# Kernel tuning notes

Hardware: AMD Instinct MI355X
Metric: run time of the kernel (lower is better)

The kernel has to match this reference:

```python
import jax, jax.numpy as jnp
import numpy as np

B, N, D = 4, 2048, 1024
G = 256          # group_size
QK = 128         # query_key_dim
H = 2048         # hidden_dim = int(dim * expansion_factor)
LN_EPS = 1e-5


def setup_inputs() -> dict:
    key = jax.random.key(0)
    ks = jax.random.split(key, 6)
    s = 0.02
    return {
        "x": jax.random.normal(ks[0], (B, N, D), jnp.float32),
        "ln_g": jnp.ones((D,), jnp.float32),
        "ln_b": jnp.zeros((D,), jnp.float32),
        "W_hidden": jax.random.normal(ks[1], (D, 2 * H), jnp.float32) * s,
        "b_hidden": jnp.zeros((2 * H,), jnp.float32),
        "W_qk": jax.random.normal(ks[2], (D, QK), jnp.float32) * s,
        "b_qk": jnp.zeros((QK,), jnp.float32),
        "os_gamma": jnp.ones((4, QK), jnp.float32) + jax.random.normal(ks[3], (4, QK), jnp.float32) * 0.02,
        "os_beta": jnp.zeros((4, QK), jnp.float32),
        "W_out": jax.random.normal(ks[4], (H, D), jnp.float32) * s,
        "b_out": jnp.zeros((D,), jnp.float32),
    }


def _rope(x):
    # x: [b, n, d]; rotary over the sequence dim, matching FLASH.rope(x, dim=1)
    n, d = x.shape[-2], x.shape[-1]
    half = d // 2
    pos = jnp.arange(n, dtype=jnp.float32)
    # freq_seq = -arange(half)/half; inv_freq = 10000 ** (-freq_seq)
    inv_freq = jnp.power(10000.0, jnp.arange(half, dtype=jnp.float32) / half)
    sinusoid = pos[:, None] * inv_freq[None, :]            # [n, half]
    sin, cos = jnp.sin(sinusoid), jnp.cos(sinusoid)
    x1, x2 = jnp.split(x, 2, axis=-1)
    return jnp.concatenate([x1 * cos - x2 * sin, x2 * cos + x1 * sin], axis=-1)


def reference(x, ln_g, ln_b, W_hidden, b_hidden, W_qk, b_qk,
              os_gamma, os_beta, W_out, b_out):
    b, n, d = x.shape
    g = G
    # LayerNorm (biased variance, as torch)
    mu = jnp.mean(x, -1, keepdims=True)
    var = jnp.mean(jnp.square(x - mu), -1, keepdims=True)
    normed = (x - mu) / jnp.sqrt(var + LN_EPS) * ln_g + ln_b

    h = jax.nn.silu(normed @ W_hidden + b_hidden)          # [b, n, 2H]
    v, gate = jnp.split(h, 2, axis=-1)                     # [b, n, H] each
    qk = jax.nn.silu(normed @ W_qk + b_qk)                 # [b, n, QK]

    # OffsetScale: 4 heads -> quad_q, lin_q, quad_k, lin_k
    qk4 = qk[..., None, :] * os_gamma + os_beta            # [b, n, 4, QK]
    quad_q, lin_q, quad_k, lin_k = (_rope(qk4[..., i, :]) for i in range(4))

    pad = (-n) % g
    if pad:
        padf = lambda t: jnp.pad(t, ((0, 0), (0, pad), (0, 0)))
        quad_q, quad_k, lin_q, lin_k, v_p = map(padf, (quad_q, quad_k, lin_q, lin_k, v))
    else:
        v_p = v
    grp = lambda t: t.reshape(b, -1, g, t.shape[-1])       # b (g n) d -> b g n d
    quad_q, quad_k, lin_q, lin_k, vg = map(grp, (quad_q, quad_k, lin_q, lin_k, v_p))

    # group-local quadratic attention with ReLU^2
    sim = jnp.einsum('bgid,bgjd->bgij', quad_q, quad_k) / g
    attn = jnp.square(jax.nn.relu(sim))
    quad_out = jnp.einsum('bgij,bgje->bgie', attn, vg)

    # linear global attention (reduced over groups), divided by full seq len n
    lin_kv = jnp.einsum('bgnd,bgne->bde', lin_k, vg) / n
    lin_out = jnp.einsum('bgnd,bde->bgne', lin_q, lin_kv)

    out = (quad_out + lin_out).reshape(b, -1, vg.shape[-1])[:, :n]
    out = gate * out
    return out @ W_out + b_out + x
```

## Files before the change

### kernel.cpp

```cpp
#include <hip/hip_runtime.h>
#include <stdint.h>

typedef __attribute__((ext_vector_type(8))) short bf16x8_t;
typedef __attribute__((ext_vector_type(4))) float f32x4_t;

#define DI __device__ __forceinline__
#define SBAR() asm volatile("s_barrier" ::: "memory")
#define VMW(n) asm volatile("s_waitcnt vmcnt(" #n ")" ::: "memory")

DI unsigned short f2b(float f) {
  union { float f; unsigned int u; } c; c.f = f;
  unsigned int u = c.u + 0x7FFFu + ((c.u >> 16) & 1u);
  return (unsigned short)(u >> 16);
}
DI unsigned int pack2(float lo, float hi) {
  return (unsigned int)f2b(lo) | ((unsigned int)f2b(hi) << 16);
}
DI float b2f(unsigned short h) {
  union { unsigned int u; float f; } c; c.u = ((unsigned int)h) << 16;
  return c.f;
}
DI float silu_f(float z) { return z / (1.0f + __expf(-z)); }

DI void load_lds16(const unsigned short* g, unsigned short* l) {
  __builtin_amdgcn_global_load_lds(
      (const __attribute__((address_space(1))) unsigned int*)g,
      (__attribute__((address_space(3))) unsigned int*)l,
      16, 0, 0);
}

struct PrepP {
  const float *Wh, *Wo, *Wqk, *x, *g, *b;
  unsigned short *WT, *WoT, *normed;
};

__global__ __launch_bounds__(256) void prep_kernel(PrepP p) {
  const int blk = blockIdx.x;
  const int tx = threadIdx.x & 31, ty = threadIdx.x >> 5;
  if (blk < 6272) {
    const float* in; unsigned short* out; int R, C, gx;
    if (blk < 4096)      { in = p.Wh;  out = p.WT;                 R = 1024; C = 4096; gx = blk; }
    else if (blk < 6144) { in = p.Wo;  out = p.WoT;                R = 2048; C = 1024; gx = blk - 4096; }
    else                 { in = p.Wqk; out = p.WT + 4096 * 1024;   R = 1024; C = 128;  gx = blk - 6144; }
    const int xTiles = C >> 5;
    const int c0 = (gx % xTiles) * 32, r0 = (gx / xTiles) * 32;
    __shared__ float tile[32][33];
#pragma unroll
    for (int i = 0; i < 4; ++i)
      tile[ty + 8 * i][tx] = in[(long)(r0 + ty + 8 * i) * C + c0 + tx];
    __syncthreads();
#pragma unroll
    for (int i = 0; i < 4; ++i)
      out[(long)(c0 + ty + 8 * i) * R + r0 + tx] = f2b(tile[tx][ty + 8 * i]);
  } else {
    const int row = blk - 6272, tid = threadIdx.x;
    __shared__ float red[8];
    float4 v = ((const float4*)(p.x + (long)row * 1024))[tid];
    float s = v.x + v.y + v.z + v.w;
    float ss = v.x * v.x + v.y * v.y + v.z * v.z + v.w * v.w;
    for (int o = 32; o > 0; o >>= 1) { s += __shfl_down(s, o); ss += __shfl_down(ss, o); }
    const int wave = tid >> 6, lane = tid & 63;
    if (lane == 0) { red[wave * 2] = s; red[wave * 2 + 1] = ss; }
    __syncthreads();
    if (tid == 0) {
      float S = red[0] + red[2] + red[4] + red[6];
      float SS = red[1] + red[3] + red[5] + red[7];
      float mu = S * (1.0f / 1024.0f);
      float var = SS * (1.0f / 1024.0f) - mu * mu;
      red[0] = mu; red[1] = rsqrtf(var + 1e-5f);
    }
    __syncthreads();
    const float mu = red[0], rstd = red[1];
    float4 gg = ((const float4*)p.g)[tid];
    float4 bb = ((const float4*)p.b)[tid];
    ushort4 o;
    o.x = f2b((v.x - mu) * rstd * gg.x + bb.x);
    o.y = f2b((v.y - mu) * rstd * gg.y + bb.y);
    o.z = f2b((v.z - mu) * rstd * gg.z + bb.z);
    o.w = f2b((v.w - mu) * rstd * gg.w + bb.w);
    ((ushort4*)(p.normed + (long)row * 1024))[tid] = o;
  }
}

__global__ __launch_bounds__(256) void reduce_cvt(
    const unsigned short* __restrict__ part, unsigned short* __restrict__ out) {
  const int idx = blockIdx.x * 256 + threadIdx.x;
  const int b = idx >> 16, i = idx & 65535;
  float4 s = make_float4(0.f, 0.f, 0.f, 0.f);
#pragma unroll
  for (int sl = 0; sl < 8; ++sl) {
    ushort4 v = ((const ushort4*)part)[(long)(b * 8 + sl) * 65536 + i];
    s.x += b2f(v.x); s.y += b2f(v.y); s.z += b2f(v.z); s.w += b2f(v.w);
  }
  ushort4 o;
  o.x = f2b(s.x); o.y = f2b(s.y); o.z = f2b(s.z); o.w = f2b(s.w);
  ((ushort4*)out)[(long)b * 65536 + i] = o;
}

struct G8P {
  const unsigned short* A;
  const unsigned short* B;
  const float* bias;
  const float* bias2;
  const float* gamma;
  const float* beta;
  unsigned short* vTout;
  unsigned short* gateOut;
  unsigned short* qqO;
  unsigned short* lqO;
  unsigned short* qkhO;
  unsigned short* lkTO;
};

__global__ __launch_bounds__(512, 2) void gemm8p(G8P p) {
  extern __shared__ unsigned char lds[];
  const int tid  = threadIdx.x;
  const int lane = tid & 63;
  const int wave = tid >> 6;
  const bool qk = blockIdx.x < 32;
  int bx, by;
  if (qk) { bx = blockIdx.x; by = 16; }
  else    { const int vg = blockIdx.x - 32; bx = vg >> 4; by = vg & 15; }
  const int wm = (wave & 1) * 128;
  const int wn = (wave >> 1) * 64;
  const int lm = lane & 15;
  const int kb = lane >> 4;

  const int rA  = tid >> 2;
  const int kby = ((tid & 3) << 4) ^ (((rA >> 1) & 3) << 4);
  const unsigned short* gA0 = p.A + (long)(bx * 256 + rA) * 1024 + (kby >> 1);
  const unsigned short* gA1 = gA0 + 128 * 1024;
  const unsigned short* gB0 = p.B + (long)(by * 256 + rA) * 1024 + (kby >> 1);
  const unsigned short* gB1 = gB0 + 128 * 1024;

  const int fxor = (kb << 4) ^ (((lm >> 1) & 3) << 4);

  f32x4_t acc[8][4];
#pragma unroll
  for (int i = 0; i < 8; ++i)
#pragma unroll
    for (int j = 0; j < 4; ++j) acc[i][j] = (f32x4_t){0.f, 0.f, 0.f, 0.f};

  auto stageA = [&](int t) {
    unsigned short* l = (unsigned short*)(lds + (t & 3) * 32768 + wave * 1024);
    load_lds16(gA0 + t * 32, l);
    load_lds16(gA1 + t * 32, (unsigned short*)((unsigned char*)l + 8192));
  };
  auto stageB = [&](int t) {
    unsigned short* l = (unsigned short*)(lds + (t & 3) * 32768 + 16384 + wave * 1024);
    load_lds16(gB0 + t * 32, l);
    load_lds16(gB1 + t * 32, (unsigned short*)((unsigned char*)l + 8192));
  };

#pragma unroll
  for (int u = 0; u < 3; ++u) { stageA(u); stageB(u); }
  VMW(8);
  SBAR();

  constexpr int NT = 16;
#pragma unroll 1
  for (int t = 0; t < NT; ++t) {
    const unsigned char* slot = lds + (t & 3) * 32768;
    bf16x8_t bF[4], aF[4];
#pragma unroll
    for (int j = 0; j < 4; ++j)
      bF[j] = *(const bf16x8_t*)(slot + 16384 + (wn + j * 16 + lm) * 64 + fxor);
#pragma unroll
    for (int i = 0; i < 4; ++i)
      aF[i] = *(const bf16x8_t*)(slot + (wm + i * 16 + lm) * 64 + fxor);
    if (t <= NT - 4) stageA(t + 3);
    SBAR();
    __builtin_amdgcn_s_setprio(1);
#pragma unroll
    for (int i = 0; i < 4; ++i)
#pragma unroll
      for (int j = 0; j < 4; ++j)
        acc[i][j] = __builtin_amdgcn_mfma_f32_16x16x32_bf16(aF[i], bF[j], acc[i][j], 0, 0, 0);
    __builtin_amdgcn_s_setprio(0);
    SBAR();
#pragma unroll
    for (int i = 0; i < 4; ++i)
      aF[i] = *(const bf16x8_t*)(slot + (wm + 64 + i * 16 + lm) * 64 + fxor);
    if (t <= NT - 4) stageB(t + 3);
    SBAR();
    __builtin_amdgcn_s_setprio(1);
#pragma unroll
    for (int i = 0; i < 4; ++i)
#pragma unroll
      for (int j = 0; j < 4; ++j)
        acc[i + 4][j] = __builtin_amdgcn_mfma_f32_16x16x32_bf16(aF[i], bF[j], acc[i + 4][j], 0, 0, 0);
    __builtin_amdgcn_s_setprio(0);
    if (t <= NT - 4)      { VMW(8); }
    else if (t == NT - 3) { VMW(4); }
    else if (t == NT - 2) { VMW(0); }
    SBAR();
  }

  if (qk) {
    unsigned short* q16 = (unsigned short*)lds;
    if (wave < 4) {
#pragma unroll
      for (int i = 0; i < 8; ++i) {
        const int rloc = wm + i * 16 + (lane >> 4) * 4;
#pragma unroll
        for (int j = 0; j < 4; ++j) {
          const int cl = wn + j * 16 + lm;
          const float bb = p.bias2[cl];
#pragma unroll
          for (int r = 0; r < 4; ++r)
            q16[(rloc + r) * 136 + cl] = f2b(silu_f(acc[i][j][r] + bb));
        }
      }
    }
    __syncthreads();
    const int j = tid & 63;
    const int rq = tid >> 6;
    const float freq = powf(10000.0f, (float)j * (1.0f / 64.0f));
    float ga[4], gb[4], ea[4], eb[4];
#pragma unroll
    for (int h = 0; h < 4; ++h) {
      ga[h] = p.gamma[h * 128 + j];  gb[h] = p.gamma[h * 128 + 64 + j];
      ea[h] = p.beta[h * 128 + j];   eb[h] = p.beta[h * 128 + 64 + j];
    }
    unsigned short* outs[3] = {p.qqO, p.lqO, p.qkhO};
    for (int rr = 0; rr < 32; ++rr) {
      const int row = rr * 8 + rq;
      const float x1 = b2f(q16[row * 136 + j]);
      const float x2 = b2f(q16[row * 136 + 64 + j]);
      const int tok = bx * 256 + row;
      const int pos = tok & 2047, bidx = tok >> 11;
      const float ang = (float)pos * freq;
      const float sn = sinf(ang), cs = cosf(ang);
#pragma unroll
      for (int h = 0; h < 3; ++h) {
        const float y1 = x1 * ga[h] + ea[h], y2 = x2 * gb[h] + eb[h];
        outs[h][(long)tok * 128 + j] = f2b(y1 * cs - y2 * sn);
        outs[h][(long)tok * 128 + 64 + j] = f2b(y2 * cs + y1 * sn);
      }
      const float y1 = x1 * ga[3] + ea[3], y2 = x2 * gb[3] + eb[3];
      p.lkTO[((long)bidx * 128 + j) * 2048 + pos] = f2b(y1 * cs - y2 * sn);
      p.lkTO[((long)bidx * 128 + 64 + j) * 2048 + pos] = f2b(y2 * cs + y1 * sn);
    }
  } else if (by < 8) {
    unsigned int* Cx = (unsigned int*)lds;
#pragma unroll
    for (int i = 0; i < 8; ++i) {
      const int c0 = (wm + i * 16) / 2 + (lane >> 4) * 2;
#pragma unroll
      for (int j = 0; j < 4; ++j) {
        const int e = wn + j * 16 + lm;
        const float bb = p.bias[by * 256 + e];
        const float s0 = silu_f(acc[i][j][0] + bb);
        const float s1 = silu_f(acc[i][j][1] + bb);
        const float s2 = silu_f(acc[i][j][2] + bb);
        const float s3 = silu_f(acc[i][j][3] + bb);
        const int x = (e & 7) << 2;
        Cx[e * 128 + (c0 ^ x)]     = pack2(s0, s1);
        Cx[e * 128 + (c0 ^ x) + 1] = pack2(s2, s3);
      }
    }
    __syncthreads();
    const int bq = bx >> 3, nloc0 = (bx & 7) * 256, e0g = by * 256;
    unsigned short* dstBase = p.vTout + ((long)(bq * 2048 + e0g)) * 2048 + nloc0;
#pragma unroll
    for (int rep = 0; rep < 16; ++rep) {
      const int flat = rep * 512 + tid;
      const int e = flat >> 5, q = flat & 31;
      uint4 val = *(const uint4*)(Cx + e * 128 + ((q ^ (e & 7)) << 2));
      *(uint4*)(dstBase + (long)e * 2048 + q * 8) = val;
    }
  } else {
#pragma unroll
    for (int i = 0; i < 8; ++i) {
      const int row0 = bx * 256 + wm + i * 16 + (lane >> 4) * 4;
#pragma unroll
      for (int j = 0; j < 4; ++j) {
        const int colg = by * 256 + wn + j * 16 + lm;
        const float bb = p.bias[colg];
#pragma unroll
        for (int r = 0; r < 4; ++r)
          p.gateOut[(long)(row0 + r) * 2048 + colg - 2048] =
              f2b(silu_f(acc[i][j][r] + bb));
      }
    }
  }
}

struct GQLP {
  const unsigned short* attn;
  const unsigned short* vT;
  const unsigned short* lq;
  const unsigned short* lkvT;
  const unsigned short* gateIn;
  unsigned short* outU;
};

__global__ __launch_bounds__(512, 2) void gemmQL(GQLP p) {
  extern __shared__ unsigned char lds[];
  const int tid  = threadIdx.x;
  const int lane = tid & 63;
  const int wave = tid >> 6;
  const int z  = blockIdx.x >> 3;
  const int by = blockIdx.x & 7;
  const int b = z >> 3, g = z & 7;
  const int wm = (wave & 1) * 128;
  const int wn = (wave >> 1) * 64;
  const int lm = lane & 15;
  const int kb = lane >> 4;

  const int rA  = tid >> 2;
  const int kby = ((tid & 3) << 4) ^ (((rA >> 1) & 3) << 4);
  const int swz = kby >> 1;
  const unsigned short* a1 = p.attn + (long)z * 65536 + rA * 256 + swz;
  const unsigned short* a2 = p.lq + ((long)z * 256 + rA) * 128 + swz;
  const unsigned short* b1 = p.vT + (long)b * 4194304 + (long)(by * 256 + rA) * 2048 + g * 256 + swz;
  const unsigned short* b2 = p.lkvT + (long)b * 262144 + (by * 256 + rA) * 128 + swz;
  const int fxor = (kb << 4) ^ (((lm >> 1) & 3) << 4);

  f32x4_t acc[8][4];
#pragma unroll
  for (int i = 0; i < 8; ++i)
#pragma unroll
    for (int j = 0; j < 4; ++j) acc[i][j] = (f32x4_t){0.f, 0.f, 0.f, 0.f};

  auto stageA = [&](int tt) {
    unsigned short* l  = (unsigned short*)(lds + (tt & 3) * 32768 + wave * 1024);
    unsigned short* lh = (unsigned short*)(lds + (tt & 3) * 32768 + wave * 1024 + 8192);
    if (tt < 8) { load_lds16(a1 + tt * 32, l); load_lds16(a1 + 128 * 256 + tt * 32, lh); }
    else { const int k2 = (tt - 8) * 32;
           load_lds16(a2 + k2, l); load_lds16(a2 + 128 * 128 + k2, lh); }
  };
  auto stageB = [&](int tt) {
    unsigned short* l  = (unsigned short*)(lds + (tt & 3) * 32768 + 16384 + wave * 1024);
    unsigned short* lh = (unsigned short*)(lds + (tt & 3) * 32768 + 16384 + wave * 1024 + 8192);
    if (tt < 8) { load_lds16(b1 + tt * 32, l); load_lds16(b1 + 128 * 2048 + tt * 32, lh); }
    else { const int k2 = (tt - 8) * 32;
           load_lds16(b2 + k2, l); load_lds16(b2 + 128 * 128 + k2, lh); }
  };

#pragma unroll
  for (int u = 0; u < 3; ++u) { stageA(u); stageB(u); }
  VMW(8);
  SBAR();

  constexpr int NT = 12;
#pragma unroll 1
  for (int t = 0; t < NT; ++t) {
    const unsigned char* slot = lds + (t & 3) * 32768;
    bf16x8_t bF[4], aF[4];
#pragma unroll
    for (int j = 0; j < 4; ++j)
      bF[j] = *(const bf16x8_t*)(slot + 16384 + (wn + j * 16 + lm) * 64 + fxor);
#pragma unroll
    for (int i = 0; i < 4; ++i)
      aF[i] = *(const bf16x8_t*)(slot + (wm + i * 16 + lm) * 64 + fxor);
    if (t <= NT - 4) stageA(t + 3);
    SBAR();
    __builtin_amdgcn_s_setprio(1);
#pragma unroll
    for (int i = 0; i < 4; ++i)
#pragma unroll
      for (int j = 0; j < 4; ++j)
        acc[i][j] = __builtin_amdgcn_mfma_f32_16x16x32_bf16(aF[i], bF[j], acc[i][j], 0, 0, 0);
    __builtin_amdgcn_s_setprio(0);
    SBAR();
#pragma unroll
    for (int i = 0; i < 4; ++i)
      aF[i] = *(const bf16x8_t*)(slot + (wm + 64 + i * 16 + lm) * 64 + fxor);
    if (t <= NT - 4) stageB(t + 3);
    SBAR();
    __builtin_amdgcn_s_setprio(1);
#pragma unroll
    for (int i = 0; i < 4; ++i)
#pragma unroll
      for (int j = 0; j < 4; ++j)
        acc[i + 4][j] = __builtin_amdgcn_mfma_f32_16x16x32_bf16(aF[i], bF[j], acc[i + 4][j], 0, 0, 0);
    __builtin_amdgcn_s_setprio(0);
    if (t <= NT - 4)      { VMW(8); }
    else if (t == NT - 3) { VMW(4); }
    else if (t == NT - 2) { VMW(0); }
    SBAR();
  }

#pragma unroll
  for (int i = 0; i < 8; ++i) {
    const int row0 = z * 256 + wm + i * 16 + (lane >> 4) * 4;
#pragma unroll
    for (int j = 0; j < 4; ++j) {
      const int col = by * 256 + wn + j * 16 + lm;
#pragma unroll
      for (int r = 0; r < 4; ++r) {
        const long idx = (long)(row0 + r) * 2048 + col;
        p.outU[idx] = f2b(b2f(p.gateIn[idx]) * acc[i][j][r]);
      }
    }
  }
}

struct GWoP {
  const unsigned short* A;
  const unsigned short* B;
  const float* bias;
  const float* xres;
  float* outF;
};

__global__ __launch_bounds__(512, 2) void gemmWo(GWoP p) {
  extern __shared__ unsigned char lds[];
  const int tid  = threadIdx.x;
  const int lane = tid & 63;
  const int wave = tid >> 6;
  const int bx = blockIdx.x >> 3;
  const int by = blockIdx.x & 7;
  const int wm = (wave & 1) * 128;
  const int wn = (wave >> 1) * 32;
  const int lm = lane & 15;
  const int kb = lane >> 4;

  const int rA  = tid >> 2;
  const int kby = ((tid & 3) << 4) ^ (((rA >> 1) & 3) << 4);
  const unsigned short* gA0 = p.A + (long)(bx * 256 + rA) * 2048 + (kby >> 1);
  const unsigned short* gA1 = gA0 + 128 * 2048;
  const unsigned short* gB0 = p.B + (long)(by * 128 + rA) * 2048 + (kby >> 1);
  const int fxor = (kb << 4) ^ (((lm >> 1) & 3) << 4);

  f32x4_t acc[8][2];
#pragma unroll
  for (int i = 0; i < 8; ++i)
#pragma unroll
    for (int j = 0; j < 2; ++j) acc[i][j] = (f32x4_t){0.f, 0.f, 0.f, 0.f};

  auto stageA = [&](int t) {
    unsigned short* l = (unsigned short*)(lds + (t & 3) * 24576 + wave * 1024);
    load_lds16(gA0 + t * 32, l);
    load_lds16(gA1 + t * 32, (unsigned short*)((unsigned char*)l + 8192));
  };
  auto stageB = [&](int t) {
    unsigned short* l = (unsigned short*)(lds + (t & 3) * 24576 + 16384 + wave * 1024);
    load_lds16(gB0 + t * 32, l);
  };

#pragma unroll
  for (int u = 0; u < 3; ++u) { stageA(u); stageB(u); }
  VMW(6);
  SBAR();

  constexpr int NT = 64;
#pragma unroll 1
  for (int t = 0; t < NT; ++t) {
    const unsigned char* slot = lds + (t & 3) * 24576;
    bf16x8_t bF[2], aF[4];
#pragma unroll
    for (int j = 0; j < 2; ++j)
      bF[j] = *(const bf16x8_t*)(slot + 16384 + (wn + j * 16 + lm) * 64 + fxor);
#pragma unroll
    for (int i = 0; i < 4; ++i)
      aF[i] = *(const bf16x8_t*)(slot + (wm + i * 16 + lm) * 64 + fxor);
    if (t <= NT - 4) stageA(t + 3);
    SBAR();
    __builtin_amdgcn_s_setprio(1);
#pragma unroll
    for (int i = 0; i < 4; ++i)
#pragma unroll
      for (int j = 0; j < 2; ++j)
        acc[i][j] = __builtin_amdgcn_mfma_f32_16x16x32_bf16(aF[i], bF[j], acc[i][j], 0, 0, 0);
    __builtin_amdgcn_s_setprio(0);
    SBAR();
#pragma unroll
    for (int i = 0; i < 4; ++i)
      aF[i] = *(const bf16x8_t*)(slot + (wm + 64 + i * 16 + lm) * 64 + fxor);
    if (t <= NT - 4) stageB(t + 3);
    SBAR();
    __builtin_amdgcn_s_setprio(1);
#pragma unroll
    for (int i = 0; i < 4; ++i)
#pragma unroll
      for (int j = 0; j < 2; ++j)
        acc[i + 4][j] = __builtin_amdgcn_mfma_f32_16x16x32_bf16(aF[i], bF[j], acc[i + 4][j], 0, 0, 0);
    __builtin_amdgcn_s_setprio(0);
    if (t <= NT - 4)      { VMW(6); }
    else if (t == NT - 3) { VMW(3); }
    else if (t == NT - 2) { VMW(0); }
    SBAR();
  }

#pragma unroll
  for (int i = 0; i < 8; ++i) {
    const int row0 = bx * 256 + wm + i * 16 + (lane >> 4) * 4;
#pragma unroll
    for (int j = 0; j < 2; ++j) {
      const int col = by * 128 + wn + j * 16 + lm;
      const float bb = p.bias[col];
#pragma unroll
      for (int r = 0; r < 4; ++r) {
        const long idx = (long)(row0 + r) * 1024 + col;
        p.outF[idx] = acc[i][j][r] + bb + p.xres[idx];
      }
    }
  }
}

enum { EPI_ARELU, EPI_PART };

struct GemmP {
  const unsigned short* A;
  const unsigned short* B;
  int K, lda, ldb, ldc, mPerZ;
  long aZ, bZ;
  float scale;
  unsigned short* outU;
};

template <int EPI>
__global__ __launch_bounds__(256, 2) void gemm_bt(GemmP p) {
  __shared__ __align__(16) unsigned char smem[16384];
  unsigned short* As = (unsigned short*)smem;
  unsigned short* Bs = (unsigned short*)(smem + 8192);

  const int tid = threadIdx.x;
  const int lane = tid & 63;
  const int wave = tid >> 6;
  const int bx = blockIdx.x;
  const int by = blockIdx.y;
  const int z = blockIdx.z;

  unsigned short* lA = As + wave * 32 * 32;
  unsigned short* lB = Bs + wave * 32 * 32;
  const int wm = (wave & 1) * 64;
  const int wn = (wave >> 1) * 64;
  const int lm = lane & 15;
  const int kb = lane >> 4;
  const int rowSel = (wave * 32 + (lane >> 2));
  const int colSel = (lane & 3) * 8;

  f32x4_t acc[4][4];
#pragma unroll
  for (int i = 0; i < 4; ++i)
#pragma unroll
    for (int j = 0; j < 4; ++j) acc[i][j] = (f32x4_t){0.f, 0.f, 0.f, 0.f};

  auto kloop = [&](const unsigned short* Ag, const unsigned short* Bg,
                   int lda, int ldb, int ksteps) {
    const int a16 = 16 * lda, b16 = 16 * ldb;
    for (int kt = 0; kt < ksteps; ++kt) {
      load_lds16(Ag, lA);
      load_lds16(Ag + a16, lA + 512);
      load_lds16(Bg, lB);
      load_lds16(Bg + b16, lB + 512);
      Ag += 32; Bg += 32;
      __syncthreads();
      bf16x8_t aF[4], bF[4];
#pragma unroll
      for (int i = 0; i < 4; ++i)
        aF[i] = *(const bf16x8_t*)(As + (wm + i * 16 + lm) * 32 + kb * 8);
#pragma unroll
      for (int j = 0; j < 4; ++j)
        bF[j] = *(const bf16x8_t*)(Bs + (wn + j * 16 + lm) * 32 + kb * 8);
#pragma unroll
      for (int i = 0; i < 4; ++i)
#pragma unroll
        for (int j = 0; j < 4; ++j)
          acc[i][j] = __builtin_amdgcn_mfma_f32_16x16x32_bf16(aF[i], bF[j], acc[i][j], 0, 0, 0);
      __syncthreads();
    }
  };

  if constexpr (EPI == EPI_PART) {
    const int b = z >> 3, s = z & 7;
    kloop(p.A + (long)b * p.aZ + s * 256 + (long)(bx * 128 + rowSel) * p.lda + colSel,
          p.B + (long)b * p.bZ + s * 256 + (long)(by * 128 + rowSel) * p.ldb + colSel,
          p.lda, p.ldb, p.K >> 5);
  } else {
    kloop(p.A + (long)z * p.aZ + (long)(bx * 128 + rowSel) * p.lda + colSel,
          p.B + (long)z * p.bZ + (long)(by * 128 + rowSel) * p.ldb + colSel,
          p.lda, p.ldb, p.K >> 5);
  }

#pragma unroll
  for (int i = 0; i < 4; ++i) {
    const int row0 = bx * 128 + wm + i * 16 + (lane >> 4) * 4;
    long rowg0;
    if constexpr (EPI == EPI_PART) rowg0 = row0;
    else rowg0 = (long)z * p.mPerZ + row0;
#pragma unroll
    for (int j = 0; j < 4; ++j) {
      const int col = by * 128 + wn + j * 16 + lm;
      if constexpr (EPI == EPI_ARELU) {
#pragma unroll
        for (int r = 0; r < 4; ++r) {
          float s = acc[i][j][r] * p.scale;
          s = s > 0.f ? s : 0.f;
          p.outU[(rowg0 + r) * (long)p.ldc + col] = f2b(s * s);
        }
      } else {
        unsigned short* slab = p.outU + (long)z * 262144;
#pragma unroll
        for (int r = 0; r < 4; ++r)
          slab[(rowg0 + r) * (long)p.ldc + col] = f2b(acc[i][j][r] * p.scale);
      }
    }
  }
}

extern "C" void kernel_launch(void* const* d_in, const int* in_sizes, int n_in,
                              void* d_out, int out_size, void* d_ws, size_t ws_size,
                              hipStream_t stream) {
  const float* x        = (const float*)d_in[0];
  const float* ln_g     = (const float*)d_in[1];
  const float* ln_b     = (const float*)d_in[2];
  const float* W_hidden = (const float*)d_in[3];
  const float* b_hidden = (const float*)d_in[4];
  const float* W_qk     = (const float*)d_in[5];
  const float* b_qk     = (const float*)d_in[6];
  const float* os_gamma = (const float*)d_in[7];
  const float* os_beta  = (const float*)d_in[8];
  const float* W_out    = (const float*)d_in[9];
  const float* b_out    = (const float*)d_in[10];
  float* out = (float*)d_out;

  char* w = (char*)d_ws;
  auto ws = [&](size_t bytes) { char* p = w; w += bytes; return (unsigned short*)p; };
  unsigned short* WT     = ws(8650752);
  unsigned short* WoT    = ws(4194304);
  unsigned short* normed = ws(16777216);
  unsigned short* vT     = ws(33554432);
  unsigned short* gate   = ws(33554432);
  unsigned short* qq     = ws(2097152);
  unsigned short* qkh    = ws(2097152);
  unsigned short* lq     = ws(2097152);
  unsigned short* lkT    = ws(2097152);
  unsigned short* attn   = ws(4194304);
  unsigned short* lkvP   = ws(16777216);
  unsigned short* lkvT   = ws(2097152);
  unsigned short* A3     = ws(33554432);

  static bool s_attr = false;
  if (!s_attr) {
    hipFuncSetAttribute((const void*)gemm8p,
                        hipFuncAttributeMaxDynamicSharedMemorySize, 131072);
    hipFuncSetAttribute((const void*)gemmQL,
                        hipFuncAttributeMaxDynamicSharedMemorySize, 131072);
    hipFuncSetAttribute((const void*)gemmWo,
                        hipFuncAttributeMaxDynamicSharedMemorySize, 98304);
    s_attr = true;
  }

  {
    PrepP p{W_hidden, W_out, W_qk, x, ln_g, ln_b, WT, WoT, normed};
    prep_kernel<<<14464, 256, 0, stream>>>(p);
  }
  {
    G8P p{normed, WT, b_hidden, b_qk, os_gamma, os_beta,
          vT, gate, qq, lq, qkh, lkT};
    gemm8p<<<dim3(544, 1, 1), 512, 131072, stream>>>(p);
  }
  {
    GemmP p{}; p.A = qq; p.B = qkh; p.K = 128; p.lda = 128; p.ldb = 128;
    p.ldc = 256; p.mPerZ = 256; p.aZ = 32768; p.bZ = 32768;
    p.scale = 1.f / 256.f; p.outU = attn;
    gemm_bt<EPI_ARELU><<<dim3(2, 2, 32), 256, 0, stream>>>(p);
  }
  {
    GemmP p{}; p.A = vT; p.B = lkT; p.K = 256; p.lda = 2048; p.ldb = 2048;
    p.ldc = 128; p.mPerZ = 2048; p.aZ = 4194304; p.bZ = 262144;
    p.scale = 1.f / 2048.f; p.outU = lkvP;
    gemm_bt<EPI_PART><<<dim3(16, 1, 32), 256, 0, stream>>>(p);
  }
  reduce_cvt<<<1024, 256, 0, stream>>>(lkvP, lkvT);
  {
    GQLP p{attn, vT, lq, lkvT, gate, A3};
    gemmQL<<<dim3(256, 1, 1), 512, 131072, stream>>>(p);
  }
  {
    GWoP p{A3, WoT, b_out, x, out};
    gemmWo<<<dim3(256, 1, 1), 512, 98304, stream>>>(p);
  }
}
```

Measured before the change: 327.0 us.

## Fuse quad-attention scores into projection GEMM via flag wait; swizzle block order

Removes the separate ReLU² attention-score kernel launch. The score tiles are computed by 128 extra blocks appended to the fused projection GEMM, and these blocks spin on a global counter until the 32 qk blocks have written their outputs. The counter is reset by an extra block in the prep kernel. Block-index remappings are also added in the projection, gemmQL and gemmWo kernels to change the tile traversal order for cache locality. The spin-wait relies on the qk blocks being scheduled before or alongside the waiting blocks, which risks deadlock or idle CUs.

```diff
diff --git a/kernel.cpp b/kernel.cpp
--- a/kernel.cpp
+++ b/kernel.cpp
@@ -32,10 +32,15 @@
 struct PrepP {
   const float *Wh, *Wo, *Wqk, *x, *g, *b;
   unsigned short *WT, *WoT, *normed;
+  unsigned int* flag;
 };
 
 __global__ __launch_bounds__(256) void prep_kernel(PrepP p) {
   const int blk = blockIdx.x;
+  if (blk >= 14464) {
+    if (threadIdx.x == 0) *p.flag = 0u;
+    return;
+  }
   const int tx = threadIdx.x & 31, ty = threadIdx.x >> 5;
   if (blk < 6272) {
     const float* in; unsigned short* out; int R, C, gx;
@@ -110,6 +115,8 @@
   unsigned short* lqO;
   unsigned short* qkhO;
   unsigned short* lkTO;
+  unsigned short* attnO;
+  unsigned int* flag;
 };
 
 __global__ __launch_bounds__(512, 2) void gemm8p(G8P p) {
@@ -117,14 +124,80 @@
   const int tid  = threadIdx.x;
   const int lane = tid & 63;
   const int wave = tid >> 6;
+  const int lm = lane & 15;
+  const int kb = lane >> 4;
+  const int fxor = (kb << 4) ^ (((lm >> 1) & 3) << 4);
+
+  if (blockIdx.x >= 544) {
+    const int az = blockIdx.x - 544;
+    const int zz = az >> 2;
+    const int bq = (az >> 1) & 1, bn = az & 1;
+    if (tid == 0) {
+      while (atomicAdd(p.flag, 0u) < 32u) __builtin_amdgcn_s_sleep(2);
+    }
+    __syncthreads();
+    __threadfence();
+    const int r128 = tid >> 2;
+    const int kby2 = ((tid & 3) << 4) ^ (((r128 >> 1) & 3) << 4);
+    const unsigned short* gq = p.qqO  + ((long)zz * 256 + bq * 128 + r128) * 128 + (kby2 >> 1);
+    const unsigned short* gk = p.qkhO + ((long)zz * 256 + bn * 128 + r128) * 128 + (kby2 >> 1);
+#pragma unroll
+    for (int kt = 0; kt < 4; ++kt) {
+      load_lds16(gq + kt * 32, (unsigned short*)(lds + kt * 8192 + wave * 1024));
+      load_lds16(gk + kt * 32, (unsigned short*)(lds + 32768 + kt * 8192 + wave * 1024));
+    }
+    VMW(0);
+    __syncthreads();
+    const int wm2 = (wave & 1) * 64;
+    const int wn2 = (wave >> 1) * 32;
+    f32x4_t ac[4][2];
+#pragma unroll
+    for (int i = 0; i < 4; ++i)
+#pragma unroll
+      for (int j = 0; j < 2; ++j) ac[i][j] = (f32x4_t){0.f, 0.f, 0.f, 0.f};
+#pragma unroll
+    for (int kt = 0; kt < 4; ++kt) {
+      bf16x8_t aF2[4], bF2[2];
+#pragma unroll
+      for (int i = 0; i < 4; ++i)
+        aF2[i] = *(const bf16x8_t*)(lds + kt * 8192 + (wm2 + i * 16 + lm) * 64 + fxor);
+#pragma unroll
+      for (int j = 0; j < 2; ++j)
+        bF2[j] = *(const bf16x8_t*)(lds + 32768 + kt * 8192 + (wn2 + j * 16 + lm) * 64 + fxor);
+#pragma unroll
+      for (int i = 0; i < 4; ++i)
+#pragma unroll
+        for (int j = 0; j < 2; ++j)
+          ac[i][j] = __builtin_amdgcn_mfma_f32_16x16x32_bf16(aF2[i], bF2[j], ac[i][j], 0, 0, 0);
+    }
+    unsigned short* outA = p.attnO + (long)zz * 65536;
+#pragma unroll
+    for (int i = 0; i < 4; ++i) {
+      const int row0 = bq * 128 + wm2 + i * 16 + (lane >> 4) * 4;
+#pragma unroll
+      for (int j = 0; j < 2; ++j) {
+        const int col = bn * 128 + wn2 + j * 16 + lm;
+#pragma unroll
+        for (int r = 0; r < 4; ++r) {
+          float s = ac[i][j][r] * (1.0f / 256.0f);
+          s = s > 0.f ? s : 0.f;
+          outA[(row0 + r) * 256 + col] = f2b(s * s);
+        }
+      }
+    }
+    return;
+  }
+
   const bool qk = blockIdx.x < 32;
   int bx, by;
   if (qk) { bx = blockIdx.x; by = 16; }
-  else    { const int vg = blockIdx.x - 32; bx = vg >> 4; by = vg & 15; }
+  else {
+    const int vg = blockIdx.x - 32;
+    const int vgs = (vg & 7) * 64 + (vg >> 3);
+    bx = vgs >> 4; by = vgs & 15;
+  }
   const int wm = (wave & 1) * 128;
   const int wn = (wave >> 1) * 64;
-  const int lm = lane & 15;
-  const int kb = lane >> 4;
 
   const int rA  = tid >> 2;
   const int kby = ((tid & 3) << 4) ^ (((rA >> 1) & 3) << 4);
@@ -132,8 +205,6 @@
   const unsigned short* gA1 = gA0 + 128 * 1024;
   const unsigned short* gB0 = p.B + (long)(by * 256 + rA) * 1024 + (kby >> 1);
   const unsigned short* gB1 = gB0 + 128 * 1024;
-
-  const int fxor = (kb << 4) ^ (((lm >> 1) & 3) << 4);
 
   f32x4_t acc[8][4];
 #pragma unroll
@@ -241,6 +312,9 @@
       p.lkTO[((long)bidx * 128 + j) * 2048 + pos] = f2b(y1 * cs - y2 * sn);
       p.lkTO[((long)bidx * 128 + 64 + j) * 2048 + pos] = f2b(y2 * cs + y1 * sn);
     }
+    __threadfence();
+    __syncthreads();
+    if (tid == 0) atomicAdd(p.flag, 1u);
   } else if (by < 8) {
     unsigned int* Cx = (unsigned int*)lds;
 #pragma unroll
@@ -300,8 +374,9 @@
   const int tid  = threadIdx.x;
   const int lane = tid & 63;
   const int wave = tid >> 6;
-  const int z  = blockIdx.x >> 3;
-  const int by = blockIdx.x & 7;
+  const int sb = (blockIdx.x & 7) * 32 + (blockIdx.x >> 3);
+  const int z  = sb >> 3;
+  const int by = sb & 7;
   const int b = z >> 3, g = z & 7;
   const int wm = (wave & 1) * 128;
   const int wn = (wave >> 1) * 64;
@@ -410,8 +485,9 @@
   const int tid  = threadIdx.x;
   const int lane = tid & 63;
   const int wave = tid >> 6;
-  const int bx = blockIdx.x >> 3;
-  const int by = blockIdx.x & 7;
+  const int sb = (blockIdx.x & 7) * 32 + (blockIdx.x >> 3);
+  const int bx = sb >> 3;
+  const int by = sb & 7;
   const int wm = (wave & 1) * 128;
   const int wn = (wave >> 1) * 32;
   const int lm = lane & 15;
@@ -500,19 +576,16 @@
   }
 }
 
-enum { EPI_ARELU, EPI_PART };
-
 struct GemmP {
   const unsigned short* A;
   const unsigned short* B;
-  int K, lda, ldb, ldc, mPerZ;
+  int K, lda, ldb, ldc;
   long aZ, bZ;
   float scale;
   unsigned short* outU;
 };
 
-template <int EPI>
-__global__ __launch_bounds__(256, 2) void gemm_bt(GemmP p) {
+__global__ __launch_bounds__(256, 2) void gemm_part(GemmP p) {
   __shared__ __align__(16) unsigned char smem[16384];
   unsigned short* As = (unsigned short*)smem;
   unsigned short* Bs = (unsigned short*)(smem + 8192);
@@ -539,65 +612,42 @@
 #pragma unroll
     for (int j = 0; j < 4; ++j) acc[i][j] = (f32x4_t){0.f, 0.f, 0.f, 0.f};
 
-  auto kloop = [&](const unsigned short* Ag, const unsigned short* Bg,
-                   int lda, int ldb, int ksteps) {
-    const int a16 = 16 * lda, b16 = 16 * ldb;
-    for (int kt = 0; kt < ksteps; ++kt) {
-      load_lds16(Ag, lA);
-      load_lds16(Ag + a16, lA + 512);
-      load_lds16(Bg, lB);
-      load_lds16(Bg + b16, lB + 512);
-      Ag += 32; Bg += 32;
-      __syncthreads();
-      bf16x8_t aF[4], bF[4];
-#pragma unroll
-      for (int i = 0; i < 4; ++i)
-        aF[i] = *(const bf16x8_t*)(As + (wm + i * 16 + lm) * 32 + kb * 8);
+  const int b = z >> 3, s = z & 7;
+  const unsigned short* Ag = p.A + (long)b * p.aZ + s * 256 + (long)(bx * 128 + rowSel) * p.lda + colSel;
+  const unsigned short* Bg = p.B + (long)b * p.bZ + s * 256 + (long)(by * 128 + rowSel) * p.ldb + colSel;
+  const int a16 = 16 * p.lda, b16 = 16 * p.ldb;
+  for (int kt = 0; kt < (p.K >> 5); ++kt) {
+    load_lds16(Ag, lA);
+    load_lds16(Ag + a16, lA + 512);
+    load_lds16(Bg, lB);
+    load_lds16(Bg + b16, lB + 512);
+    Ag += 32; Bg += 32;
+    __syncthreads();
+    bf16x8_t aF[4], bF[4];
+#pragma unroll
+    for (int i = 0; i < 4; ++i)
+      aF[i] = *(const bf16x8_t*)(As + (wm + i * 16 + lm) * 32 + kb * 8);
+#pragma unroll
+    for (int j = 0; j < 4; ++j)
+      bF[j] = *(const bf16x8_t*)(Bs + (wn + j * 16 + lm) * 32 + kb * 8);
+#pragma unroll
+    for (int i = 0; i < 4; ++i)
 #pragma unroll
       for (int j = 0; j < 4; ++j)
-        bF[j] = *(const bf16x8_t*)(Bs + (wn + j * 16 + lm) * 32 + kb * 8);
-#pragma unroll
-      for (int i = 0; i < 4; ++i)
-#pragma unroll
-        for (int j = 0; j < 4; ++j)
-          acc[i][j] = __builtin_amdgcn_mfma_f32_16x16x32_bf16(aF[i], bF[j], acc[i][j], 0, 0, 0);
-      __syncthreads();
-    }
-  };
-
-  if constexpr (EPI == EPI_PART) {
-    const int b = z >> 3, s = z & 7;
-    kloop(p.A + (long)b * p.aZ + s * 256 + (long)(bx * 128 + rowSel) * p.lda + colSel,
-          p.B + (long)b * p.bZ + s * 256 + (long)(by * 128 + rowSel) * p.ldb + colSel,
-          p.lda, p.ldb, p.K >> 5);
-  } else {
-    kloop(p.A + (long)z * p.aZ + (long)(bx * 128 + rowSel) * p.lda + colSel,
-          p.B + (long)z * p.bZ + (long)(by * 128 + rowSel) * p.ldb + colSel,
-          p.lda, p.ldb, p.K >> 5);
+        acc[i][j] = __builtin_amdgcn_mfma_f32_16x16x32_bf16(aF[i], bF[j], acc[i][j], 0, 0, 0);
+    __syncthreads();
   }
 
 #pragma unroll
   for (int i = 0; i < 4; ++i) {
     const int row0 = bx * 128 + wm + i * 16 + (lane >> 4) * 4;
-    long rowg0;
-    if constexpr (EPI == EPI_PART) rowg0 = row0;
-    else rowg0 = (long)z * p.mPerZ + row0;
 #pragma unroll
     for (int j = 0; j < 4; ++j) {
       const int col = by * 128 + wn + j * 16 + lm;
-      if constexpr (EPI == EPI_ARELU) {
-#pragma unroll
-        for (int r = 0; r < 4; ++r) {
-          float s = acc[i][j][r] * p.scale;
-          s = s > 0.f ? s : 0.f;
-          p.outU[(rowg0 + r) * (long)p.ldc + col] = f2b(s * s);
-        }
-      } else {
-        unsigned short* slab = p.outU + (long)z * 262144;
-#pragma unroll
-        for (int r = 0; r < 4; ++r)
-          slab[(rowg0 + r) * (long)p.ldc + col] = f2b(acc[i][j][r] * p.scale);
-      }
+      unsigned short* slab = p.outU + (long)z * 262144;
+#pragma unroll
+      for (int r = 0; r < 4; ++r)
+        slab[(row0 + r) * (long)p.ldc + col] = f2b(acc[i][j][r] * p.scale);
     }
   }
 }
@@ -633,6 +683,7 @@
   unsigned short* lkvP   = ws(16777216);
   unsigned short* lkvT   = ws(2097152);
   unsigned short* A3     = ws(33554432);
+  unsigned int*   flag   = (unsigned int*)ws(256);
 
   static bool s_attr = false;
   if (!s_attr) {
@@ -646,25 +697,19 @@
   }
 
   {
-    PrepP p{W_hidden, W_out, W_qk, x, ln_g, ln_b, WT, WoT, normed};
-    prep_kernel<<<14464, 256, 0, stream>>>(p);
+    PrepP p{W_hidden, W_out, W_qk, x, ln_g, ln_b, WT, WoT, normed, flag};
+    prep_kernel<<<14465, 256, 0, stream>>>(p);
   }
   {
     G8P p{normed, WT, b_hidden, b_qk, os_gamma, os_beta,
-          vT, gate, qq, lq, qkh, lkT};
-    gemm8p<<<dim3(544, 1, 1), 512, 131072, stream>>>(p);
-  }
-  {
-    GemmP p{}; p.A = qq; p.B = qkh; p.K = 128; p.lda = 128; p.ldb = 128;
-    p.ldc = 256; p.mPerZ = 256; p.aZ = 32768; p.bZ = 32768;
-    p.scale = 1.f / 256.f; p.outU = attn;
-    gemm_bt<EPI_ARELU><<<dim3(2, 2, 32), 256, 0, stream>>>(p);
+          vT, gate, qq, lq, qkh, lkT, attn, flag};
+    gemm8p<<<dim3(672, 1, 1), 512, 131072, stream>>>(p);
   }
   {
     GemmP p{}; p.A = vT; p.B = lkT; p.K = 256; p.lda = 2048; p.ldb = 2048;
-    p.ldc = 128; p.mPerZ = 2048; p.aZ = 4194304; p.bZ = 262144;
+    p.ldc = 128; p.aZ = 4194304; p.bZ = 262144;
     p.scale = 1.f / 2048.f; p.outU = lkvP;
-    gemm_bt<EPI_PART><<<dim3(16, 1, 32), 256, 0, stream>>>(p);
+    gemm_part<<<dim3(16, 1, 32), 256, 0, stream>>>(p);
   }
   reduce_cvt<<<1024, 256, 0, stream>>>(lkvP, lkvT);
   {
```

Result: slower. 354.2 us (+8.3%).

## Retile gemmQL to 256x128 tiles with triple buffering and drop redundant barriers

Applied to the files above, without the earlier changes.

The gemmQL kernel is retiled from 256x256 to 256x128 output tiles. This doubles the grid to 512 blocks, cuts LDS to 72KB with a 3-slot ring at prefetch distance 2, and raises launch bounds to 4 blocks per CU, aiming for better occupancy and load balance. The two mid-iteration s_barriers in the gemm8p, gemmQL and gemmWo main loops are removed, relying on the end-of-iteration barrier and the fact that prefetch targets a slot no longer being read. The gemm_bt k-loop lambda is inlined, which is a cleanup. The trade-offs are less B-operand reuse per block and looser wave synchronisation, which could change LDS contention.

```diff
diff --git a/kernel.cpp b/kernel.cpp
--- a/kernel.cpp
+++ b/kernel.cpp
@@ -169,7 +169,6 @@
     for (int i = 0; i < 4; ++i)
       aF[i] = *(const bf16x8_t*)(slot + (wm + i * 16 + lm) * 64 + fxor);
     if (t <= NT - 4) stageA(t + 3);
-    SBAR();
     __builtin_amdgcn_s_setprio(1);
 #pragma unroll
     for (int i = 0; i < 4; ++i)
@@ -177,12 +176,10 @@
       for (int j = 0; j < 4; ++j)
         acc[i][j] = __builtin_amdgcn_mfma_f32_16x16x32_bf16(aF[i], bF[j], acc[i][j], 0, 0, 0);
     __builtin_amdgcn_s_setprio(0);
-    SBAR();
 #pragma unroll
     for (int i = 0; i < 4; ++i)
       aF[i] = *(const bf16x8_t*)(slot + (wm + 64 + i * 16 + lm) * 64 + fxor);
     if (t <= NT - 4) stageB(t + 3);
-    SBAR();
     __builtin_amdgcn_s_setprio(1);
 #pragma unroll
     for (int i = 0; i < 4; ++i)
@@ -295,16 +292,16 @@
   unsigned short* outU;
 };
 
-__global__ __launch_bounds__(512, 2) void gemmQL(GQLP p) {
+__global__ __launch_bounds__(512, 4) void gemmQL(GQLP p) {
   extern __shared__ unsigned char lds[];
   const int tid  = threadIdx.x;
   const int lane = tid & 63;
   const int wave = tid >> 6;
-  const int z  = blockIdx.x >> 3;
-  const int by = blockIdx.x & 7;
+  const int z  = blockIdx.x >> 4;
+  const int by = blockIdx.x & 15;
   const int b = z >> 3, g = z & 7;
   const int wm = (wave & 1) * 128;
-  const int wn = (wave >> 1) * 64;
+  const int wn = (wave >> 1) * 32;
   const int lm = lane & 15;
   const int kb = lane >> 4;
 
@@ -313,71 +310,66 @@
   const int swz = kby >> 1;
   const unsigned short* a1 = p.attn + (long)z * 65536 + rA * 256 + swz;
   const unsigned short* a2 = p.lq + ((long)z * 256 + rA) * 128 + swz;
-  const unsigned short* b1 = p.vT + (long)b * 4194304 + (long)(by * 256 + rA) * 2048 + g * 256 + swz;
-  const unsigned short* b2 = p.lkvT + (long)b * 262144 + (by * 256 + rA) * 128 + swz;
+  const unsigned short* b1 = p.vT + (long)b * 4194304 + (long)(by * 128 + rA) * 2048 + g * 256 + swz;
+  const unsigned short* b2 = p.lkvT + (long)b * 262144 + (by * 128 + rA) * 128 + swz;
   const int fxor = (kb << 4) ^ (((lm >> 1) & 3) << 4);
 
-  f32x4_t acc[8][4];
+  f32x4_t acc[8][2];
 #pragma unroll
   for (int i = 0; i < 8; ++i)
 #pragma unroll
-    for (int j = 0; j < 4; ++j) acc[i][j] = (f32x4_t){0.f, 0.f, 0.f, 0.f};
+    for (int j = 0; j < 2; ++j) acc[i][j] = (f32x4_t){0.f, 0.f, 0.f, 0.f};
 
   auto stageA = [&](int tt) {
-    unsigned short* l  = (unsigned short*)(lds + (tt & 3) * 32768 + wave * 1024);
-    unsigned short* lh = (unsigned short*)(lds + (tt & 3) * 32768 + wave * 1024 + 8192);
+    unsigned char* base = lds + (tt % 3) * 24576;
+    unsigned short* l  = (unsigned short*)(base + wave * 1024);
+    unsigned short* lh = (unsigned short*)(base + wave * 1024 + 8192);
     if (tt < 8) { load_lds16(a1 + tt * 32, l); load_lds16(a1 + 128 * 256 + tt * 32, lh); }
     else { const int k2 = (tt - 8) * 32;
            load_lds16(a2 + k2, l); load_lds16(a2 + 128 * 128 + k2, lh); }
   };
   auto stageB = [&](int tt) {
-    unsigned short* l  = (unsigned short*)(lds + (tt & 3) * 32768 + 16384 + wave * 1024);
-    unsigned short* lh = (unsigned short*)(lds + (tt & 3) * 32768 + 16384 + wave * 1024 + 8192);
-    if (tt < 8) { load_lds16(b1 + tt * 32, l); load_lds16(b1 + 128 * 2048 + tt * 32, lh); }
-    else { const int k2 = (tt - 8) * 32;
-           load_lds16(b2 + k2, l); load_lds16(b2 + 128 * 128 + k2, lh); }
+    unsigned short* l = (unsigned short*)(lds + (tt % 3) * 24576 + 16384 + wave * 1024);
+    if (tt < 8) load_lds16(b1 + tt * 32, l);
+    else        load_lds16(b2 + (tt - 8) * 32, l);
   };
 
 #pragma unroll
-  for (int u = 0; u < 3; ++u) { stageA(u); stageB(u); }
-  VMW(8);
+  for (int u = 0; u < 2; ++u) { stageA(u); stageB(u); }
+  VMW(3);
   SBAR();
 
   constexpr int NT = 12;
 #pragma unroll 1
   for (int t = 0; t < NT; ++t) {
-    const unsigned char* slot = lds + (t & 3) * 32768;
-    bf16x8_t bF[4], aF[4];
-#pragma unroll
-    for (int j = 0; j < 4; ++j)
+    const unsigned char* slot = lds + (t % 3) * 24576;
+    bf16x8_t bF[2], aF[4];
+#pragma unroll
+    for (int j = 0; j < 2; ++j)
       bF[j] = *(const bf16x8_t*)(slot + 16384 + (wn + j * 16 + lm) * 64 + fxor);
 #pragma unroll
     for (int i = 0; i < 4; ++i)
       aF[i] = *(const bf16x8_t*)(slot + (wm + i * 16 + lm) * 64 + fxor);
-    if (t <= NT - 4) stageA(t + 3);
-    SBAR();
+    if (t <= NT - 3) stageA(t + 2);
     __builtin_amdgcn_s_setprio(1);
 #pragma unroll
     for (int i = 0; i < 4; ++i)
 #pragma unroll
-      for (int j = 0; j < 4; ++j)
+      for (int j = 0; j < 2; ++j)
         acc[i][j] = __builtin_amdgcn_mfma_f32_16x16x32_bf16(aF[i], bF[j], acc[i][j], 0, 0, 0);
     __builtin_amdgcn_s_setprio(0);
-    SBAR();
 #pragma unroll
     for (int i = 0; i < 4; ++i)
       aF[i] = *(const bf16x8_t*)(slot + (wm + 64 + i * 16 + lm) * 64 + fxor);
-    if (t <= NT - 4) stageB(t + 3);
-    SBAR();
+    if (t <= NT - 3) stageB(t + 2);
     __builtin_amdgcn_s_setprio(1);
 #pragma unroll
     for (int i = 0; i < 4; ++i)
 #pragma unroll
-      for (int j = 0; j < 4; ++j)
+      for (int j = 0; j < 2; ++j)
         acc[i + 4][j] = __builtin_amdgcn_mfma_f32_16x16x32_bf16(aF[i], bF[j], acc[i + 4][j], 0, 0, 0);
     __builtin_amdgcn_s_setprio(0);
-    if (t <= NT - 4)      { VMW(8); }
-    else if (t == NT - 3) { VMW(4); }
+    if (t <= NT - 3)      { VMW(3); }
     else if (t == NT - 2) { VMW(0); }
     SBAR();
   }
@@ -386,8 +378,8 @@
   for (int i = 0; i < 8; ++i) {
     const int row0 = z * 256 + wm + i * 16 + (lane >> 4) * 4;
 #pragma unroll
-    for (int j = 0; j < 4; ++j) {
-      const int col = by * 256 + wn + j * 16 + lm;
+    for (int j = 0; j < 2; ++j) {
+      const int col = by * 128 + wn + j * 16 + lm;
 #pragma unroll
       for (int r = 0; r < 4; ++r) {
         const long idx = (long)(row0 + r) * 2048 + col;
@@ -457,7 +449,6 @@
     for (int i = 0; i < 4; ++i)
       aF[i] = *(const bf16x8_t*)(slot + (wm + i * 16 + lm) * 64 + fxor);
     if (t <= NT - 4) stageA(t + 3);
-    SBAR();
     __builtin_amdgcn_s_setprio(1);
 #pragma unroll
     for (int i = 0; i < 4; ++i)
@@ -465,12 +456,10 @@
       for (int j = 0; j < 2; ++j)
         acc[i][j] = __builtin_amdgcn_mfma_f32_16x16x32_bf16(aF[i], bF[j], acc[i][j], 0, 0, 0);
     __builtin_amdgcn_s_setprio(0);
-    SBAR();
 #pragma unroll
     for (int i = 0; i < 4; ++i)
       aF[i] = *(const bf16x8_t*)(slot + (wm + 64 + i * 16 + lm) * 64 + fxor);
     if (t <= NT - 4) stageB(t + 3);
-    SBAR();
     __builtin_amdgcn_s_setprio(1);
 #pragma unroll
     for (int i = 0; i < 4; ++i)
@@ -539,41 +528,37 @@
 #pragma unroll
     for (int j = 0; j < 4; ++j) acc[i][j] = (f32x4_t){0.f, 0.f, 0.f, 0.f};
 
-  auto kloop = [&](const unsigned short* Ag, const unsigned short* Bg,
-                   int lda, int ldb, int ksteps) {
-    const int a16 = 16 * lda, b16 = 16 * ldb;
-    for (int kt = 0; kt < ksteps; ++kt) {
-      load_lds16(Ag, lA);
-      load_lds16(Ag + a16, lA + 512);
-      load_lds16(Bg, lB);
-      load_lds16(Bg + b16, lB + 512);
-      Ag += 32; Bg += 32;
-      __syncthreads();
-      bf16x8_t aF[4], bF[4];
-#pragma unroll
-      for (int i = 0; i < 4; ++i)
-        aF[i] = *(const bf16x8_t*)(As + (wm + i * 16 + lm) * 32 + kb * 8);
-#pragma unroll
-      for (int j = 0; j < 4; ++j)
-        bF[j] = *(const bf16x8_t*)(Bs + (wn + j * 16 + lm) * 32 + kb * 8);
-#pragma unroll
-      for (int i = 0; i < 4; ++i)
-#pragma unroll
-        for (int j = 0; j < 4; ++j)
-          acc[i][j] = __builtin_amdgcn_mfma_f32_16x16x32_bf16(aF[i], bF[j], acc[i][j], 0, 0, 0);
-      __syncthreads();
-    }
-  };
-
+  const unsigned short* Ag;
+  const unsigned short* Bg;
   if constexpr (EPI == EPI_PART) {
     const int b = z >> 3, s = z & 7;
-    kloop(p.A + (long)b * p.aZ + s * 256 + (long)(bx * 128 + rowSel) * p.lda + colSel,
-          p.B + (long)b * p.bZ + s * 256 + (long)(by * 128 + rowSel) * p.ldb + colSel,
-          p.lda, p.ldb, p.K >> 5);
+    Ag = p.A + (long)b * p.aZ + s * 256 + (long)(bx * 128 + rowSel) * p.lda + colSel;
+    Bg = p.B + (long)b * p.bZ + s * 256 + (long)(by * 128 + rowSel) * p.ldb + colSel;
   } else {
-    kloop(p.A + (long)z * p.aZ + (long)(bx * 128 + rowSel) * p.lda + colSel,
-          p.B + (long)z * p.bZ + (long)(by * 128 + rowSel) * p.ldb + colSel,
-          p.lda, p.ldb, p.K >> 5);
+    Ag = p.A + (long)z * p.aZ + (long)(bx * 128 + rowSel) * p.lda + colSel;
+    Bg = p.B + (long)z * p.bZ + (long)(by * 128 + rowSel) * p.ldb + colSel;
+  }
+  const int a16 = 16 * p.lda, b16 = 16 * p.ldb;
+  for (int kt = 0; kt < (p.K >> 5); ++kt) {
+    load_lds16(Ag, lA);
+    load_lds16(Ag + a16, lA + 512);
+    load_lds16(Bg, lB);
+    load_lds16(Bg + b16, lB + 512);
+    Ag += 32; Bg += 32;
+    __syncthreads();
+    bf16x8_t aF[4], bF[4];
+#pragma unroll
+    for (int i = 0; i < 4; ++i)
+      aF[i] = *(const bf16x8_t*)(As + (wm + i * 16 + lm) * 32 + kb * 8);
+#pragma unroll
+    for (int j = 0; j < 4; ++j)
+      bF[j] = *(const bf16x8_t*)(Bs + (wn + j * 16 + lm) * 32 + kb * 8);
+#pragma unroll
+    for (int i = 0; i < 4; ++i)
+#pragma unroll
+      for (int j = 0; j < 4; ++j)
+        acc[i][j] = __builtin_amdgcn_mfma_f32_16x16x32_bf16(aF[i], bF[j], acc[i][j], 0, 0, 0);
+    __syncthreads();
   }
 
 #pragma unroll
@@ -639,7 +624,7 @@
     hipFuncSetAttribute((const void*)gemm8p,
                         hipFuncAttributeMaxDynamicSharedMemorySize, 131072);
     hipFuncSetAttribute((const void*)gemmQL,
-                        hipFuncAttributeMaxDynamicSharedMemorySize, 131072);
+                        hipFuncAttributeMaxDynamicSharedMemorySize, 73728);
     hipFuncSetAttribute((const void*)gemmWo,
                         hipFuncAttributeMaxDynamicSharedMemorySize, 98304);
     s_attr = true;
@@ -662,14 +647,14 @@
   }
   {
     GemmP p{}; p.A = vT; p.B = lkT; p.K = 256; p.lda = 2048; p.ldb = 2048;
-    p.ldc = 128; p.mPerZ = 2048; p.aZ = 4194304; p.bZ = 262144;
+    p.ldc = 128; p.aZ = 4194304; p.bZ = 262144;
     p.scale = 1.f / 2048.f; p.outU = lkvP;
     gemm_bt<EPI_PART><<<dim3(16, 1, 32), 256, 0, stream>>>(p);
   }
   reduce_cvt<<<1024, 256, 0, stream>>>(lkvP, lkvT);
   {
     GQLP p{attn, vT, lq, lkvT, gate, A3};
-    gemmQL<<<dim3(256, 1, 1), 512, 131072, stream>>>(p);
+    gemmQL<<<dim3(512, 1, 1), 512, 73728, stream>>>(p);
   }
   {
     GWoP p{A3, WoT, b_out, x, out};
```

Measured after the change: 314.7 us. 1.04x faster.
